# Performance work log

Hardware: AMD Instinct MI355X
Metric: run time of the kernel (lower is better)

## Reference

```python
import jax, jax.numpy as jnp
import numpy as np

# Model dims: batch, seq, d_model, heads, layers, vocab, ffn, max_distance
B, S, D, H, L, V, F, M = 2, 1024, 1024, 16, 6, 32000, 4096, 1024
Dh = D // H


def setup_inputs() -> dict:
    key = jax.random.key(0)
    ks = jax.random.split(key, 24)
    std = 0.02
    w = lambda k, shape: (jax.random.normal(k, shape, jnp.float32) * std)
    return {
        "tokens": jax.random.randint(ks[0], (B, S), 0, V, jnp.int32),
        "emb": w(ks[1], (V, D)),
        "Wq": w(ks[2], (L, D, D)), "bq": jnp.zeros((L, D), jnp.float32),
        "Wk": w(ks[3], (L, D, D)), "bk": jnp.zeros((L, D), jnp.float32),
        "Wv": w(ks[4], (L, D, D)), "bv": jnp.zeros((L, D), jnp.float32),
        "Wo": w(ks[5], (L, D, D)), "bo": jnp.zeros((L, D), jnp.float32),
        "rpe": w(ks[6], (L, M, Dh)),  # per-layer key-RPE embedding table
        "ln1_s": jnp.ones((L, D), jnp.float32), "ln1_b": jnp.zeros((L, D), jnp.float32),
        "ln2_s": jnp.ones((L, D), jnp.float32), "ln2_b": jnp.zeros((L, D), jnp.float32),
        "W1": w(ks[7], (L, D, F)), "b1": jnp.zeros((L, F), jnp.float32),
        "W2": w(ks[8], (L, F, D)), "b2": jnp.zeros((L, D), jnp.float32),
        "Wout": w(ks[9], (D, V)), "bout": jnp.zeros((V,), jnp.float32),
    }


def _ln(x, s, b):
    mu = jnp.mean(x, -1, keepdims=True)
    var = jnp.mean((x - mu) ** 2, -1, keepdims=True)
    return (x - mu) * jax.lax.rsqrt(var + 1e-5) * s + b


def _forward(tokens, emb, Wq, bq, Wk, bk, Wv, bv, Wo, bo, rpe,
             ln1_s, ln1_b, ln2_s, ln2_b, W1, b1, W2, b2, Wout, bout):
    x = emb[tokens]  # (B, S, D); dropout is identity at inference
    mask = jnp.tril(jnp.ones((S, S), bool))
    inv_sqrt_d = np.float32(1.0 / np.sqrt(Dh))

    def block(x, p):
        (wq, bq_, wk, bk_, wv, bv_, wo, bo_, rp,
         l1s, l1b, l2s, l2b, w1, b1_, w2, b2_) = p
        heads = lambda W, b: (x @ W + b).reshape(B, S, H, Dh).transpose(0, 2, 1, 3)
        q, k, v = heads(wq, bq_), heads(wk, bk_), heads(wv, bv_)
        qk = jnp.einsum('bhqd,bhkd->bhqk', q, k)
        # Music-Transformer skew: srel = Q @ E^T, pad-left 1, reshape, drop first row
        srel = jnp.einsum('bhqd,md->bhqm', q, rp[-S:])  # M == S, no clipping branch
        srel = jnp.pad(srel, ((0, 0), (0, 0), (0, 0), (1, 0)))
        srel = srel.reshape(B, H, S + 1, S)[:, :, 1:, :]
        logits = (qk + srel) * inv_sqrt_d
        logits = jnp.where(mask, logits, jnp.float32(-1e9))
        wgt = jax.nn.softmax(logits, axis=-1)
        o = jnp.einsum('bhqk,bhkd->bhqd', wgt, v).transpose(0, 2, 1, 3).reshape(B, S, D)
        o = o @ wo + bo_
        x2 = _ln(x + o, l1s, l1b)           # post-LN residual (attention)
        f = jax.nn.gelu(x2 @ w1 + b1_) @ w2 + b2_
        return _ln(x2 + f, l2s, l2b), None  # post-LN residual (FFN)

    x, _ = jax.lax.scan(block, x, (Wq, bq, Wk, bk, Wv, bv, Wo, bo, rpe,
                                   ln1_s, ln1_b, ln2_s, ln2_b, W1, b1, W2, b2))
    return x @ Wout + bout  # (B, S, V)


def reference(tokens, emb, Wq, bq, Wk, bk, Wv, bv, Wo, bo, rpe,
              ln1_s, ln1_b, ln2_s, ln2_b, W1, b1, W2, b2, Wout, bout):
    return _forward(tokens, emb, Wq, bq, Wk, bk, Wv, bv, Wo, bo, rpe,
                    ln1_s, ln1_b, ln2_s, ln2_b, W1, b1, W2, b2, Wout, bout)
```

## Files before the change

### kernel.cpp

```cpp
#include <hip/hip_runtime.h>
#include <hip/hip_bf16.h>
#include <cstdint>

constexpr int NB = 2, NS = 1024, ND = 1024, NH = 16, NL = 6, NV = 32000, NF = 4096, NDH = 64;

using bf16 = __hip_bfloat16;
typedef __bf16 bf16x8 __attribute__((ext_vector_type(8)));
typedef float f32x4 __attribute__((ext_vector_type(4)));

#define AS1(p) ((const __attribute__((address_space(1))) void*)(p))
#define AS3(p) ((__attribute__((address_space(3))) void*)(p))

__device__ __forceinline__ float gelu_f(float x) {
  float z = 1.5957691216057308f * (x + 0.044715f * x * x * x);
  return x / (1.f + __expf(-z));
}

template<int EP, bool HASBIAS>
__global__ __launch_bounds__(512)
void gemm256p(const bf16* __restrict__ A, const bf16* __restrict__ Bt,
              void* __restrict__ Cv, const float* __restrict__ bias,
              int K, int lda, int ldb, int ldc)
{
  const int nM = gridDim.y, nN = gridDim.x;
  const int nwg = nM * nN;
  const int bid = blockIdx.y * nN + blockIdx.x;
  const int wg = (bid & 7) * (nwg >> 3) + (bid >> 3);
  const int m0 = (wg % nM) * 256;
  const int n0 = (wg / nM) * 256;

  __shared__ char lds[131072];

  const int tid = threadIdx.x, lane = tid & 63, wid = tid >> 6;
  const int wm = (wid >> 2) * 128;
  const int wn = (wid & 3) * 64;
  const int l15 = lane & 15, g4 = lane >> 4;
  const int rdk = (g4 * 16) ^ ((l15 >> 3) << 5);

  const int srow = wid * 16 + (lane >> 2);
  const int scol = ((lane & 3) * 8) ^ (((lane >> 5) & 1) << 4);
  const bf16* gA = A  + (long)(m0 + srow) * lda + scol;
  const bf16* gB = Bt + (long)(n0 + srow) * ldb + scol;
  const long a128 = 128l * lda, b128 = 128l * ldb;

  f32x4 acc[8][4] = {};
  const int NT = K >> 6;

#define SGA(bufsel_, t_, kc_) do {                                                     \
    char* d_ = lds + (bufsel_) * 65536 + (kc_) * 16384 + wid * 1024;                   \
    const long ko_ = (long)(t_) * 64 + (kc_) * 32;                                     \
    __builtin_amdgcn_global_load_lds(AS1(gA + ko_),        AS3(d_),        16, 0, 0);  \
    __builtin_amdgcn_global_load_lds(AS1(gA + ko_ + a128), AS3(d_ + 8192), 16, 0, 0);  \
  } while (0)
#define SGB(bufsel_, t_, kc_) do {                                                     \
    char* d_ = lds + (bufsel_) * 65536 + 32768 + (kc_) * 16384 + wid * 1024;           \
    const long ko_ = (long)(t_) * 64 + (kc_) * 32;                                     \
    __builtin_amdgcn_global_load_lds(AS1(gB + ko_),        AS3(d_),        16, 0, 0);  \
    __builtin_amdgcn_global_load_lds(AS1(gB + ko_ + b128), AS3(d_ + 8192), 16, 0, 0);  \
  } while (0)

#define PH(vm_, bufsel_, kc_, ih_, RDB_, STGX_) do {                                   \
    asm volatile("s_waitcnt vmcnt(" #vm_ ")" ::: "memory");                            \
    __builtin_amdgcn_s_barrier();                                                      \
    asm volatile("" ::: "memory");                                                     \
    const char* la_ = lds + (bufsel_) * 65536 + (kc_) * 16384;                         \
    const char* lb_ = lds + (bufsel_) * 65536 + 32768 + (kc_) * 16384;                 \
    if (RDB_) {                                                                        \
      _Pragma("unroll") for (int j_ = 0; j_ < 4; ++j_)                                 \
        bfr[j_] = *(const bf16x8*)(lb_ + (wn + j_ * 16 + l15) * 64 + rdk);             \
    }                                                                                  \
    bf16x8 af_[4];                                                                     \
    _Pragma("unroll") for (int i2_ = 0; i2_ < 4; ++i2_)                                \
      af_[i2_] = *(const bf16x8*)(la_ + (wm + (ih_) * 64 + i2_ * 16 + l15) * 64 + rdk);\
    STGX_;                                                                             \
    __builtin_amdgcn_s_setprio(1);                                                     \
    _Pragma("unroll") for (int i2_ = 0; i2_ < 4; ++i2_)                                \
      _Pragma("unroll") for (int j_ = 0; j_ < 4; ++j_)                                 \
        acc[(ih_) * 4 + i2_][j_] = __builtin_amdgcn_mfma_f32_16x16x32_bf16(            \
            af_[i2_], bfr[j_], acc[(ih_) * 4 + i2_][j_], 0, 0, 0);                     \
    __builtin_amdgcn_s_setprio(0);                                                     \
    asm volatile("" ::: "memory");                                                     \
    __builtin_amdgcn_s_barrier();                                                      \
  } while (0)

  SGB(0, 0, 0);
  SGA(0, 0, 0);
  SGB(0, 0, 1);
  SGA(0, 0, 1);
  SGB(1, 1, 0);
  SGA(1, 1, 0);
  SGB(1, 1, 1);

  for (int i = 0; i < (NT >> 1) - 1; ++i) {
    const int t1 = 2 * i + 1, t2 = 2 * i + 2, t3 = 2 * i + 3;
    bf16x8 bfr[4];
    PH(10, 0, 0, 0, 1, SGA(1, t1, 1));
    PH(12, 0, 0, 1, 0, SGB(0, t2, 0));
    PH(10, 0, 1, 0, 1, SGA(0, t2, 0));
    PH(12, 0, 1, 1, 0, SGB(0, t2, 1));
    PH(10, 1, 0, 0, 1, SGA(0, t2, 1));
    PH(12, 1, 0, 1, 0, SGB(1, t3, 0));
    PH(10, 1, 1, 0, 1, SGA(1, t3, 0));
    PH(12, 1, 1, 1, 0, SGB(1, t3, 1));
  }
  {
    const int t1 = NT - 1;
    bf16x8 bfr[4];
    PH(10, 0, 0, 0, 1, SGA(1, t1, 1));
    PH(12, 0, 0, 1, 0, (void)0);
    PH( 8, 0, 1, 0, 1, (void)0);
    PH( 8, 0, 1, 1, 0, (void)0);
    PH( 4, 1, 0, 0, 1, (void)0);
    PH( 4, 1, 0, 1, 0, (void)0);
    PH( 0, 1, 1, 0, 1, (void)0);
    PH( 0, 1, 1, 1, 0, (void)0);
  }
#undef PH
#undef SGA
#undef SGB

  const int rq = (lane >> 4) * 4;
  #pragma unroll
  for (int i = 0; i < 8; ++i) {
    const int r0 = m0 + wm + i * 16 + rq;
    #pragma unroll
    for (int j = 0; j < 4; ++j) {
      const int c = n0 + wn + j * 16 + l15;
      float bv = 0.f;
      if constexpr (HASBIAS) bv = bias[c];
      #pragma unroll
      for (int e = 0; e < 4; ++e) {
        float v = acc[i][j][e] + bv;
        if constexpr (EP == 2) v = gelu_f(v);
        if constexpr (EP == 0) ((float*)Cv)[(long)(r0 + e) * ldc + c] = v;
        else                   ((bf16*)Cv)[(long)(r0 + e) * ldc + c] = __float2bfloat16(v);
      }
    }
  }
}

template<int EP, bool HASBIAS, int KSZ>
__global__ __launch_bounds__(256)
void gemm128_bt(const bf16* __restrict__ A, const bf16* __restrict__ Bt,
                void* __restrict__ Cv, const float* __restrict__ bias,
                int K, int lda, int ldb, int ldc, long sEP)
{
  const int nM = gridDim.y, nN = gridDim.x;
  const int nwg = nM * nN;
  const int bid = blockIdx.y * nN + blockIdx.x;
  const int qq = nwg >> 3;
  const int wg = (bid & 7) * qq + (bid >> 3);
  const int m0 = (wg % nM) * 128;
  const int n0 = (wg / nM) * 256;

  const int kLen = K / KSZ;
  const long kOff = (long)blockIdx.z * kLen;

  __shared__ char lds[73728];

  const int tid  = threadIdx.x;
  const int lane = tid & 63;
  const int wid  = tid >> 6;
  const int wn   = wid * 64;
  const int l15  = lane & 15;
  const int rdk  = ((lane >> 4) * 16) ^ ((l15 >> 3) << 5);

  const int srow = wid * 16 + (lane >> 2);
  const int scol = ((lane & 3) * 8) ^ (((lane >> 5) & 1) << 4);
  const bf16* gA = A  + (long)(m0 + srow) * lda + scol + kOff;
  const bf16* gB = Bt + (long)(n0 + srow) * ldb + scol + kOff;
  const long a64 = 64l * lda, b64 = 64l * ldb;

  f32x4 acc[8][4] = {};
  const int NT = kLen >> 5;

#define STG(t_, b_) do {                                                               \
    char* dA = lds + (b_) * 24576 + wid * 1024;                                        \
    char* dB = lds + (b_) * 24576 + 8192 + wid * 1024;                                 \
    const long ko_ = (long)(t_) * 32;                                                  \
    __builtin_amdgcn_global_load_lds(AS1(gA + ko_),           AS3(dA),         16, 0, 0); \
    __builtin_amdgcn_global_load_lds(AS1(gA + ko_ + a64),     AS3(dA + 4096),  16, 0, 0); \
    __builtin_amdgcn_global_load_lds(AS1(gB + ko_),           AS3(dB),         16, 0, 0); \
    __builtin_amdgcn_global_load_lds(AS1(gB + ko_ + b64),     AS3(dB + 4096),  16, 0, 0); \
    __builtin_amdgcn_global_load_lds(AS1(gB + ko_ + 2 * b64), AS3(dB + 8192),  16, 0, 0); \
    __builtin_amdgcn_global_load_lds(AS1(gB + ko_ + 3 * b64), AS3(dB + 12288), 16, 0, 0); \
  } while (0)

#define TBODY(cur_) do {                                                               \
    const char* la_ = lds + (cur_) * 24576;                                            \
    const char* lb_ = la_ + 8192;                                                      \
    bf16x8 bf_[4], af_[8];                                                             \
    _Pragma("unroll") for (int j_ = 0; j_ < 4; ++j_)                                   \
      bf_[j_] = *(const bf16x8*)(lb_ + (wn + j_ * 16 + l15) * 64 + rdk);               \
    _Pragma("unroll") for (int i_ = 0; i_ < 8; ++i_)                                   \
      af_[i_] = *(const bf16x8*)(la_ + (i_ * 16 + l15) * 64 + rdk);                    \
    __builtin_amdgcn_s_setprio(1);                                                     \
    _Pragma("unroll") for (int i_ = 0; i_ < 8; ++i_)                                   \
      _Pragma("unroll") for (int j_ = 0; j_ < 4; ++j_)                                 \
        acc[i_][j_] = __builtin_amdgcn_mfma_f32_16x16x32_bf16(af_[i_], bf_[j_], acc[i_][j_], 0, 0, 0); \
    __builtin_amdgcn_s_setprio(0);                                                     \
  } while (0)

  STG(0, 0); STG(1, 1);
  int cur = 0, nxt = 2;
  for (int t = 0; t < NT - 1; ++t) {
    asm volatile("s_waitcnt vmcnt(6)" ::: "memory");
    __builtin_amdgcn_s_barrier();
    asm volatile("" ::: "memory");
    if (t + 2 < NT) STG(t + 2, nxt);
    TBODY(cur);
    cur = (cur == 2) ? 0 : cur + 1;
    nxt = (nxt == 2) ? 0 : nxt + 1;
  }
  asm volatile("s_waitcnt vmcnt(0)" ::: "memory");
  __builtin_amdgcn_s_barrier();
  asm volatile("" ::: "memory");
  TBODY(cur);
#undef TBODY
#undef STG

  const int rq = (lane >> 4) * 4;
  #pragma unroll
  for (int i = 0; i < 8; ++i) {
    const int r0 = m0 + i * 16 + rq;
    #pragma unroll
    for (int j = 0; j < 4; ++j) {
      const int c = n0 + wn + j * 16 + l15;
      float bv = 0.f;
      if constexpr (HASBIAS) { if (KSZ == 1 || blockIdx.z == 0) bv = bias[c]; }
      #pragma unroll
      for (int e = 0; e < 4; ++e) {
        float v = acc[i][j][e] + bv;
        if constexpr (EP == 0) {
          float* Cz = (float*)Cv + (KSZ > 1 ? (long)blockIdx.z * sEP : 0);
          Cz[(long)(r0 + e) * ldc + c] = v;
        } else if constexpr (EP == 2) {
          ((bf16*)Cv)[(long)(r0 + e) * ldc + c] = __float2bfloat16(gelu_f(v));
        } else {
          ((bf16*)Cv)[(long)(c >> 10) * sEP + (long)(r0 + e) * ND + (c & 1023)] =
              __float2bfloat16(v);
        }
      }
    }
  }
}

template<int BN, int EP, int CZ, bool HASBIAS, int SWZ, int KS>
__global__ __launch_bounds__(256)
void gemm_bt(const bf16* __restrict__ A, const bf16* __restrict__ Bt,
             void* __restrict__ Cv, const float* __restrict__ bias,
             int M, int N, int K, int lda, int ldb, int ldc, int ZH,
             long sAb, long sAh, long sBb, long sBh, long sCb, long sCh, long sBias)
{
  constexpr int BM = 128, BK = 32;
  constexpr int WGN = (BN == 128) ? 2 : 1;
  constexpr int FM  = (BM / (4 / WGN)) / 16;
  constexpr int FN  = (BN / WGN) / 16;

  const int z  = blockIdx.z;
  const int zb = z / ZH, zh = z % ZH;
  const bf16* Ab = A + (long)zb * sAb + (long)zh * sAh;
  const bf16* Bb = Bt + (long)zb * sBb + (long)zh * sBh;

  const int m0 = blockIdx.y * BM;
  const int n0 = blockIdx.x * BN;

  if constexpr (CZ == 3) { if (m0 + n0 + BM + BN - 2 < NS - 1) return; }

  __shared__ bf16 Asm[BM * BK];
  __shared__ bf16 Bsm[BN * BK];

  const int tid  = threadIdx.x;
  const int lane = tid & 63;
  const int wid  = tid >> 6;
  const int wm = (wid / WGN) * (FM * 16);
  const int wn = (wid % WGN) * (FN * 16);
  const int l15 = lane & 15;
  const int lk8 = (lane >> 4) * 8;

  f32x4 acc[FM][FN] = {};

  const int srow = tid >> 2;
  const int scol = (tid & 3) * 8;
  const bf16* gA = Ab + (long)(m0 + srow) * lda + scol;
  const bf16* gB = Bb + (long)(n0 + srow) * ldb + scol;
  bf16* ldsA = Asm + wid * 512;
  bf16* ldsB = Bsm + wid * 512;

  for (int k0 = 0; k0 < K; k0 += BK) {
    __builtin_amdgcn_global_load_lds(AS1(gA + k0), AS3(ldsA), 16, 0, 0);
    __builtin_amdgcn_global_load_lds(AS1(gA + 64l * lda + k0), AS3(ldsA + 2048), 16, 0, 0);
    __builtin_amdgcn_global_load_lds(AS1(gB + k0), AS3(ldsB), 16, 0, 0);
    if constexpr (BN == 128)
      __builtin_amdgcn_global_load_lds(AS1(gB + 64l * ldb + k0), AS3(ldsB + 2048), 16, 0, 0);
    asm volatile("s_waitcnt vmcnt(0)" ::: "memory");
    __syncthreads();

    bf16x8 af[FM], bfr[FN];
    #pragma unroll
    for (int i = 0; i < FM; ++i)
      af[i] = *reinterpret_cast<const bf16x8*>(&Asm[(wm + i * 16 + l15) * BK + lk8]);
    #pragma unroll
    for (int j = 0; j < FN; ++j)
      bfr[j] = *reinterpret_cast<const bf16x8*>(&Bsm[(wn + j * 16 + l15) * BK + lk8]);
    #pragma unroll
    for (int i = 0; i < FM; ++i)
      #pragma unroll
      for (int j = 0; j < FN; ++j)
        acc[i][j] = __builtin_amdgcn_mfma_f32_16x16x32_bf16(af[i], bfr[j], acc[i][j], 0, 0, 0);
    __syncthreads();
  }

  const int rq = (lane >> 4) * 4;
  const long cb = (long)zb * sCb + (long)zh * sCh;
  #pragma unroll
  for (int i = 0; i < FM; ++i) {
    const int r0 = m0 + wm + i * 16 + rq;
    #pragma unroll
    for (int j = 0; j < FN; ++j) {
      const int c = n0 + wn + j * 16 + l15;
      float bv = 0.f;
      if constexpr (HASBIAS) bv = bias[(long)zb * sBias + c];
      #pragma unroll
      for (int e = 0; e < 4; ++e) {
        float v = acc[i][j][e] + bv;
        const long idx = cb + (long)(r0 + e) * ldc + c;
        if constexpr (EP == 0) ((float*)Cv)[idx] = v;
        else                   ((bf16*)Cv)[idx] = __float2bfloat16(v);
      }
    }
  }
}

__global__ __launch_bounds__(256)
void flash_attn_k(const bf16* __restrict__ qkv, const bf16* __restrict__ vt,
                  const bf16* __restrict__ qe, bf16* __restrict__ ob)
{
  const int z  = blockIdx.x;
  const int qt = 15 - blockIdx.y;
  const int b  = z >> 4, h = z & 15;
  const int q0 = qt * 64;
  const int tid  = threadIdx.x;
  const int lane = tid & 63;
  const int wid  = tid >> 6;
  const int l15  = lane & 15;
  const int g4   = lane >> 4;
  const int xk   = (l15 & 7) << 4;

  __shared__ char lds[58368];
  char* Qlds = lds;
  char* Klds = lds + 8192;
  char* Vlds = lds + 24576;
  char* Plds = lds + 40960;

  const bf16* Qg  = qkv + ((long)b * NS + q0) * ND + h * 64;
  const bf16* Kg  = qkv + (long)NB * NS * ND + (long)b * NS * ND + h * 64;
  const bf16* Vg  = vt + (long)z * 64 * NS;
  const bf16* QEg = qe + (long)z * NS * NS;

  #pragma unroll
  for (int i = 0; i < 2; ++i) {
    const int slot = i * 256 + tid;
    const int r = slot >> 3, seg = slot & 7;
    const int sc = (seg ^ (r & 7)) * 8;
    __builtin_amdgcn_global_load_lds(AS1(Qg + (long)r * ND + sc),
                                     AS3(Qlds + (i * 4096 + wid * 1024)), 16, 0, 0);
  }

  f32x4 aqk[8], apv[4];
  #pragma unroll
  for (int j = 0; j < 4; ++j) apv[j] = (f32x4){0.f, 0.f, 0.f, 0.f};
  float mrun[4] = {-3e38f, -3e38f, -3e38f, -3e38f};
  float lrun[4] = {0.f, 0.f, 0.f, 0.f};

  const int nk = (q0 + 191) >> 7;

  for (int kt = 0; kt < nk; ++kt) {
    const int k0 = kt * 128;
    __builtin_amdgcn_s_barrier();

    #pragma unroll
    for (int i = 0; i < 4; ++i) {
      const int slot = i * 256 + tid;
      const int r = slot >> 3, seg = slot & 7;
      const int sc = (seg ^ (r & 7)) * 8;
      __builtin_amdgcn_global_load_lds(AS1(Kg + (long)(k0 + r) * ND + sc),
                                       AS3(Klds + (i * 4096 + wid * 1024)), 16, 0, 0);
    }
    #pragma unroll
    for (int i = 0; i < 4; ++i) {
      const int slot = i * 256 + tid;
      const int d = slot >> 4, seg = slot & 15;
      const int sc = (seg ^ (d & 7)) * 8;
      __builtin_amdgcn_global_load_lds(AS1(Vg + (long)d * NS + k0 + sc),
                                       AS3(Vlds + (i * 4096 + wid * 1024)), 16, 0, 0);
    }

    unsigned short se[4][8];
    #pragma unroll
    for (int e = 0; e < 4; ++e) {
      const int qg = q0 + wid * 16 + g4 * 4 + e;
      const long rowb = (long)qg * NS;
      #pragma unroll
      for (int f = 0; f < 8; ++f) {
        int m = 1023 - qg + k0 + 16 * f + l15;
        m = m > 1023 ? 1023 : m;
        se[e][f] = *(const unsigned short*)(QEg + rowb + m);
      }
    }

    asm volatile("s_waitcnt vmcnt(0)" ::: "memory");
    __builtin_amdgcn_s_barrier();

    #pragma unroll
    for (int f = 0; f < 8; ++f) aqk[f] = (f32x4){0.f, 0.f, 0.f, 0.f};
    #pragma unroll
    for (int ds = 0; ds < 2; ++ds) {
      const int ko = (ds * 32 + g4 * 8) * 2;
      bf16x8 a = *(const bf16x8*)(Qlds + (((wid * 16 + l15) * 128 + ko) ^ xk));
      #pragma unroll
      for (int f = 0; f < 8; ++f) {
        bf16x8 bb = *(const bf16x8*)(Klds + (((16 * f + l15) * 128 + ko) ^ xk));
        aqk[f] = __builtin_amdgcn_mfma_f32_16x16x32_bf16(a, bb, aqk[f], 0, 0, 0);
      }
    }

    float ps[4][8];
    float scl[4];
    #pragma unroll
    for (int e = 0; e < 4; ++e) {
      const int qg = q0 + wid * 16 + g4 * 4 + e;
      float s[8];
      float mx = mrun[e];
      #pragma unroll
      for (int f = 0; f < 8; ++f) {
        const int kg = k0 + 16 * f + l15;
        const float sv = __uint_as_float((unsigned)se[e][f] << 16);
        const float t = (aqk[f][e] + sv) * 0.125f;
        s[f] = (kg <= qg) ? t : -1e30f;
        mx = fmaxf(mx, s[f]);
      }
      #pragma unroll
      for (int o = 1; o < 16; o <<= 1) mx = fmaxf(mx, __shfl_xor(mx, o));
      const float sc_ = __expf(mrun[e] - mx);
      float ls = 0.f;
      #pragma unroll
      for (int f = 0; f < 8; ++f) { const float p = __expf(s[f] - mx); ps[e][f] = p; ls += p; }
      #pragma unroll
      for (int o = 1; o < 16; o <<= 1) ls += __shfl_xor(ls, o);
      lrun[e] = lrun[e] * sc_ + ls;
      mrun[e] = mx;
      scl[e] = sc_;
    }
    #pragma unroll
    for (int fd = 0; fd < 4; ++fd)
      #pragma unroll
      for (int e = 0; e < 4; ++e) apv[fd][e] *= scl[e];

    #pragma unroll
    for (int e = 0; e < 4; ++e) {
      char* pr = Plds + (wid * 16 + g4 * 4 + e) * 272 + l15 * 2;
      #pragma unroll
      for (int f = 0; f < 8; ++f)
        *(bf16*)(pr + f * 32) = __float2bfloat16(ps[e][f]);
    }
    asm volatile("s_waitcnt lgkmcnt(0)" ::: "memory");
    __builtin_amdgcn_sched_barrier(0);

    #pragma unroll
    for (int ks = 0; ks < 4; ++ks) {
      const int ko = (ks * 32 + g4 * 8) * 2;
      bf16x8 a = *(const bf16x8*)(Plds + (wid * 16 + l15) * 272 + ko);
      #pragma unroll
      for (int fd = 0; fd < 4; ++fd) {
        bf16x8 bb = *(const bf16x8*)(Vlds + (((16 * fd + l15) * 256 + ko) ^ xk));
        apv[fd] = __builtin_amdgcn_mfma_f32_16x16x32_bf16(a, bb, apv[fd], 0, 0, 0);
      }
    }
  }

  #pragma unroll
  for (int e = 0; e < 4; ++e) {
    const float rl = 1.f / lrun[e];
    const int qg = q0 + wid * 16 + g4 * 4 + e;
    bf16* orow = ob + ((long)b * NS + qg) * ND + h * 64;
    #pragma unroll
    for (int fd = 0; fd < 4; ++fd)
      orow[16 * fd + l15] = __float2bfloat16(apv[fd][e] * rl);
  }
}

__global__ void transpose64_k(const float* __restrict__ in, bf16* __restrict__ out,
                              int R, int C, long inZ, long outZ) {
  __shared__ float t[64][65];
  const float* ip = in + (long)blockIdx.z * inZ;
  bf16* op = out + (long)blockIdx.z * outZ;
  const int c0 = blockIdx.x * 64, r0 = blockIdx.y * 64;
  const int tid = threadIdx.x;
  const int lr = tid >> 4;
  const int lc = (tid & 15) * 4;
  #pragma unroll
  for (int i = 0; i < 4; ++i) {
    const float4 v = *(const float4*)(ip + (long)(r0 + lr + 16 * i) * C + c0 + lc);
    t[lr + 16 * i][lc]     = v.x;
    t[lr + 16 * i][lc + 1] = v.y;
    t[lr + 16 * i][lc + 2] = v.z;
    t[lr + 16 * i][lc + 3] = v.w;
  }
  __syncthreads();
  #pragma unroll
  for (int i = 0; i < 4; ++i) {
    const int oc = lr + 16 * i;
    ushort4 u;
    bf16 h0 = __float2bfloat16(t[lc][oc]);
    bf16 h1 = __float2bfloat16(t[lc + 1][oc]);
    bf16 h2 = __float2bfloat16(t[lc + 2][oc]);
    bf16 h3 = __float2bfloat16(t[lc + 3][oc]);
    u.x = *(unsigned short*)&h0; u.y = *(unsigned short*)&h1;
    u.z = *(unsigned short*)&h2; u.w = *(unsigned short*)&h3;
    *(ushort4*)(op + (long)(c0 + oc) * R + r0 + lc) = u;
  }
}

__global__ void transpose_v_k(const bf16* __restrict__ v, bf16* __restrict__ vt) {
  __shared__ bf16 t[32][33];
  const int z = blockIdx.z, b = z >> 4, h = z & 15;
  const bf16* ip = v + (long)b * NS * ND + h * 64;
  bf16* op = vt + (long)z * 64 * NS;
  const int s0 = blockIdx.x * 32, d0 = blockIdx.y * 32;
  const int tx = threadIdx.x, ty = threadIdx.y;
  #pragma unroll
  for (int i = 0; i < 4; ++i)
    t[ty * 4 + i][tx] = ip[(long)(s0 + ty * 4 + i) * ND + d0 + tx];
  __syncthreads();
  #pragma unroll
  for (int i = 0; i < 4; ++i)
    op[(long)(d0 + ty * 4 + i) * NS + s0 + tx] = t[tx][ty * 4 + i];
}

__global__ void cvt_bf16_k(const float* __restrict__ in, bf16* __restrict__ out, int n) {
  int i = blockIdx.x * 256 + threadIdx.x;
  if (i < n) out[i] = __float2bfloat16(in[i]);
}

__global__ void pack3_k(const float* __restrict__ a, const float* __restrict__ b,
                        const float* __restrict__ c, float* __restrict__ out) {
  int i = blockIdx.x * 256 + threadIdx.x;
  if (i >= NL * 3 * ND) return;
  int d = i % ND, r = (i / ND) % 3, l = i / (3 * ND);
  const float* src = (r == 0) ? a : ((r == 1) ? b : c);
  out[i] = src[l * ND + d];
}

__global__ void embed_k(const int* __restrict__ tok, const float* __restrict__ emb,
                        float* __restrict__ x, bf16* __restrict__ xb) {
  const int row = blockIdx.x;
  const int t = tok[row];
  const float4 val = ((const float4*)(emb + (long)t * ND))[threadIdx.x];
  ((float4*)(x + (long)row * ND))[threadIdx.x] = val;
  bf16* xp = xb + (long)row * ND + threadIdx.x * 4;
  xp[0] = __float2bfloat16(val.x); xp[1] = __float2bfloat16(val.y);
  xp[2] = __float2bfloat16(val.z); xp[3] = __float2bfloat16(val.w);
}

__global__ void resid_ln_k(float* __restrict__ x, const float* __restrict__ g,
                           long gs,
                           const float* __restrict__ s, const float* __restrict__ b,
                           bf16* __restrict__ xb) {
  const int row = blockIdx.x, tid = threadIdx.x;
  const float4 xv = ((const float4*)(x + (long)row * ND))[tid];
  const float4 ga = ((const float4*)(g + (long)row * ND))[tid];
  const float4 gb = ((const float4*)(g + gs + (long)row * ND))[tid];
  const float4 gc = ((const float4*)(g + 2 * gs + (long)row * ND))[tid];
  const float4 gd = ((const float4*)(g + 3 * gs + (long)row * ND))[tid];
  float h0 = xv.x + ga.x + gb.x + gc.x + gd.x;
  float h1 = xv.y + ga.y + gb.y + gc.y + gd.y;
  float h2 = xv.z + ga.z + gb.z + gc.z + gd.z;
  float h3 = xv.w + ga.w + gb.w + gc.w + gd.w;
  float ls = h0 + h1 + h2 + h3;
  __shared__ float red[8];
  #pragma unroll
  for (int o = 32; o; o >>= 1) ls += __shfl_xor(ls, o);
  const int lane = tid & 63, wid = tid >> 6;
  if (lane == 0) red[wid] = ls;
  __syncthreads();
  const float mu = (red[0] + red[1] + red[2] + red[3]) * (1.f / ND);
  const float d0 = h0 - mu, d1 = h1 - mu, d2 = h2 - mu, d3 = h3 - mu;
  float lv = d0 * d0 + d1 * d1 + d2 * d2 + d3 * d3;
  #pragma unroll
  for (int o = 32; o; o >>= 1) lv += __shfl_xor(lv, o);
  if (lane == 0) red[4 + wid] = lv;
  __syncthreads();
  const float rs = rsqrtf((red[4] + red[5] + red[6] + red[7]) * (1.f / ND) + 1e-5f);
  const float4 sv = ((const float4*)s)[tid];
  const float4 bv = ((const float4*)b)[tid];
  const float y0 = d0 * rs * sv.x + bv.x, y1 = d1 * rs * sv.y + bv.y;
  const float y2 = d2 * rs * sv.z + bv.z, y3 = d3 * rs * sv.w + bv.w;
  ((float4*)(x + (long)row * ND))[tid] = make_float4(y0, y1, y2, y3);
  bf16* xp = xb + (long)row * ND + tid * 4;
  xp[0] = __float2bfloat16(y0); xp[1] = __float2bfloat16(y1);
  xp[2] = __float2bfloat16(y2); xp[3] = __float2bfloat16(y3);
}

extern "C" void kernel_launch(void* const* d_in, const int* in_sizes, int n_in,
                              void* d_out, int out_size, void* d_ws, size_t ws_size,
                              hipStream_t stream) {
  const int*   tokens = (const int*)d_in[0];
  const float* emb  = (const float*)d_in[1];
  const float* Wq   = (const float*)d_in[2];
  const float* bq   = (const float*)d_in[3];
  const float* Wk   = (const float*)d_in[4];
  const float* bk   = (const float*)d_in[5];
  const float* Wv   = (const float*)d_in[6];
  const float* bv   = (const float*)d_in[7];
  const float* Wo   = (const float*)d_in[8];
  const float* bo   = (const float*)d_in[9];
  const float* rpe  = (const float*)d_in[10];
  const float* ln1s = (const float*)d_in[11];
  const float* ln1b = (const float*)d_in[12];
  const float* ln2s = (const float*)d_in[13];
  const float* ln2b = (const float*)d_in[14];
  const float* W1   = (const float*)d_in[15];
  const float* b1   = (const float*)d_in[16];
  const float* W2   = (const float*)d_in[17];
  const float* b2   = (const float*)d_in[18];
  const float* Wout = (const float*)d_in[19];
  const float* bout = (const float*)d_in[20];
  float* out = (float*)d_out;

  char* wsb = (char*)d_ws;
  size_t off = 0;
  auto take = [&](size_t bytes) -> void* {
    void* r = wsb + off;
    off = (off + bytes + 255) & ~(size_t)255;
    return r;
  };
  bf16*  wqkvT = (bf16*)take((size_t)NL * 3 * ND * ND * 2);
  bf16*  woT   = (bf16*)take((size_t)NL * ND * ND * 2);
  bf16*  w1T   = (bf16*)take((size_t)NL * NF * ND * 2);
  bf16*  w2T   = (bf16*)take((size_t)NL * ND * NF * 2);
  bf16*  woutT = (bf16*)take((size_t)NV * ND * 2);
  bf16*  rpeb  = (bf16*)take((size_t)NL * NS * NDH * 2);
  float* qkvb  = (float*)take((size_t)NL * 3 * ND * 4);
  float* x     = (float*)take((size_t)NB * NS * ND * 4);
  bf16*  xb    = (bf16*)take((size_t)NB * NS * ND * 2);
  bf16*  qkv   = (bf16*)take((size_t)3 * NB * NS * ND * 2);
  bf16*  vt    = (bf16*)take((size_t)NB * NS * ND * 2);
  bf16*  ob    = (bf16*)take((size_t)NB * NS * ND * 2);
  float* g     = (float*)take((size_t)4 * NB * NS * ND * 4);
  bf16*  hbuf  = (bf16*)take((size_t)NB * NS * NF * 2);
  bf16*  qe    = (bf16*)take((size_t)NB * NH * NS * NS * 2 + 4096);
  (void)in_sizes; (void)n_in; (void)out_size; (void)ws_size;

  const long gStride = (long)NB * NS * ND;

  transpose64_k<<<dim3(ND/64, ND/64, NL), 256, 0, stream>>>(Wq, wqkvT,                   ND, ND, (long)ND*ND, (long)3*ND*ND);
  transpose64_k<<<dim3(ND/64, ND/64, NL), 256, 0, stream>>>(Wk, wqkvT + (size_t)ND*ND,   ND, ND, (long)ND*ND, (long)3*ND*ND);
  transpose64_k<<<dim3(ND/64, ND/64, NL), 256, 0, stream>>>(Wv, wqkvT + (size_t)2*ND*ND, ND, ND, (long)ND*ND, (long)3*ND*ND);
  transpose64_k<<<dim3(ND/64, ND/64, NL), 256, 0, stream>>>(Wo, woT,                     ND, ND, (long)ND*ND, (long)ND*ND);
  transpose64_k<<<dim3(NF/64, ND/64, NL), 256, 0, stream>>>(W1, w1T,                     ND, NF, (long)ND*NF, (long)NF*ND);
  transpose64_k<<<dim3(ND/64, NF/64, NL), 256, 0, stream>>>(W2, w2T,                     NF, ND, (long)NF*ND, (long)ND*NF);
  transpose64_k<<<dim3(NV/64, ND/64, 1),  256, 0, stream>>>(Wout, woutT,                 ND, NV, 0, 0);
  cvt_bf16_k<<<(NL*NS*NDH + 255)/256, 256, 0, stream>>>(rpe, rpeb, NL*NS*NDH);
  pack3_k<<<(NL*3*ND + 255)/256, 256, 0, stream>>>(bq, bk, bv, qkvb);
  embed_k<<<NB*NS, 256, 0, stream>>>(tokens, emb, x, xb);

  const dim3 tb(32, 8);
  for (int l = 0; l < NL; ++l) {
    gemm128_bt<3, true, 1><<<dim3(3*ND/256, NB*NS/128), 256, 0, stream>>>(
        xb, wqkvT + (size_t)l*3*ND*ND, qkv, qkvb + (size_t)l*3*ND,
        ND, ND, ND, ND, gStride);
    transpose_v_k<<<dim3(NS/32, 2, NB*NH), tb, 0, stream>>>(qkv + (size_t)2*NB*NS*ND, vt);
    gemm_bt<128, 1, 3, false, 0, 0><<<dim3(NS/128, NS/128, NB*NH), 256, 0, stream>>>(
        qkv, rpeb + (size_t)l*NS*NDH, qe, nullptr,
        NS, NS, NDH, ND, NDH, NS, NH,
        (long)NS*ND, 64, 0, 0, (long)NH*NS*NS, (long)NS*NS, 0);
    flash_attn_k<<<dim3(NB*NH, 16), 256, 0, stream>>>(qkv, vt, qe, ob);
    gemm128_bt<0, true, 4><<<dim3(ND/256, NB*NS/128, 4), 256, 0, stream>>>(
        ob, woT + (size_t)l*ND*ND, g, bo + (size_t)l*ND, ND, ND, ND, ND, gStride);
    resid_ln_k<<<NB*NS, 256, 0, stream>>>(x, g, gStride,
        ln1s + (size_t)l*ND, ln1b + (size_t)l*ND, xb);
    gemm128_bt<2, true, 1><<<dim3(NF/256, NB*NS/128), 256, 0, stream>>>(
        xb, w1T + (size_t)l*NF*ND, hbuf, b1 + (size_t)l*NF, ND, ND, ND, NF, 0);
    gemm128_bt<0, true, 4><<<dim3(ND/256, NB*NS/128, 4), 256, 0, stream>>>(
        hbuf, w2T + (size_t)l*ND*NF, g, b2 + (size_t)l*ND, NF, NF, NF, ND, gStride);
    resid_ln_k<<<NB*NS, 256, 0, stream>>>(x, g, gStride,
        ln2s + (size_t)l*ND, ln2b + (size_t)l*ND, xb);
  }
  gemm256p<0, true><<<dim3(NV/256, NB*NS/256), 512, 0, stream>>>(
      xb, woutT, out, bout, ND, ND, ND, NV);
}
```

Before: 1.358 ms.

## Restructure GEMM into 4-stage K pipeline and register-prefetch attention K/V tiles

The main GEMM moves from a double-buffered, 8-phase 64-wide K schedule to a 4-slot ring of 32-wide K stages. Each stage loads all A and B fragments, issues the prefetch three stages ahead, and splits the MFMAs across lgkmcnt waits with one barrier per stage. The flash attention kernel now keeps Q in registers instead of LDS and prefetches the next K/V tile into registers during the current iteration, then writes it to swizzled LDS. The aim is better overlap of global loads with compute and fewer barriers, at the cost of more registers and different LDS usage.

```diff
diff --git a/kernel.cpp b/kernel.cpp
--- a/kernel.cpp
+++ b/kernel.cpp
@@ -44,80 +44,56 @@
   const long a128 = 128l * lda, b128 = 128l * ldb;
 
   f32x4 acc[8][4] = {};
-  const int NT = K >> 6;
-
-#define SGA(bufsel_, t_, kc_) do {                                                     \
-    char* d_ = lds + (bufsel_) * 65536 + (kc_) * 16384 + wid * 1024;                   \
-    const long ko_ = (long)(t_) * 64 + (kc_) * 32;                                     \
-    __builtin_amdgcn_global_load_lds(AS1(gA + ko_),        AS3(d_),        16, 0, 0);  \
-    __builtin_amdgcn_global_load_lds(AS1(gA + ko_ + a128), AS3(d_ + 8192), 16, 0, 0);  \
+  const int NP = K >> 5;
+
+#define STGP(p_) do {                                                                  \
+    const int s_ = (p_) & 3; const long ko_ = (long)(p_) * 32;                         \
+    char* dA = lds + s_ * 32768 + wid * 1024;                                          \
+    char* dB = dA + 16384;                                                             \
+    __builtin_amdgcn_global_load_lds(AS1(gA + ko_),        AS3(dA),        16, 0, 0);  \
+    __builtin_amdgcn_global_load_lds(AS1(gA + ko_ + a128), AS3(dA + 8192), 16, 0, 0);  \
+    __builtin_amdgcn_global_load_lds(AS1(gB + ko_),        AS3(dB),        16, 0, 0);  \
+    __builtin_amdgcn_global_load_lds(AS1(gB + ko_ + b128), AS3(dB + 8192), 16, 0, 0);  \
   } while (0)
-#define SGB(bufsel_, t_, kc_) do {                                                     \
-    char* d_ = lds + (bufsel_) * 65536 + 32768 + (kc_) * 16384 + wid * 1024;           \
-    const long ko_ = (long)(t_) * 64 + (kc_) * 32;                                     \
-    __builtin_amdgcn_global_load_lds(AS1(gB + ko_),        AS3(d_),        16, 0, 0);  \
-    __builtin_amdgcn_global_load_lds(AS1(gB + ko_ + b128), AS3(d_ + 8192), 16, 0, 0);  \
-  } while (0)
-
-#define PH(vm_, bufsel_, kc_, ih_, RDB_, STGX_) do {                                   \
+
+#define PAIR(vm_, p_, DOSTG_) do {                                                     \
     asm volatile("s_waitcnt vmcnt(" #vm_ ")" ::: "memory");                            \
     __builtin_amdgcn_s_barrier();                                                      \
     asm volatile("" ::: "memory");                                                     \
-    const char* la_ = lds + (bufsel_) * 65536 + (kc_) * 16384;                         \
-    const char* lb_ = lds + (bufsel_) * 65536 + 32768 + (kc_) * 16384;                 \
-    if (RDB_) {                                                                        \
+    const char* la_ = lds + ((p_) & 3) * 32768;                                        \
+    const char* lb_ = la_ + 16384;                                                     \
+    bf16x8 bfr[4], af[8];                                                              \
+    _Pragma("unroll") for (int j_ = 0; j_ < 4; ++j_)                                   \
+      bfr[j_] = *(const bf16x8*)(lb_ + (wn + j_ * 16 + l15) * 64 + rdk);               \
+    _Pragma("unroll") for (int i_ = 0; i_ < 4; ++i_)                                   \
+      af[i_] = *(const bf16x8*)(la_ + (wm + i_ * 16 + l15) * 64 + rdk);                \
+    __builtin_amdgcn_sched_barrier(0);                                                 \
+    _Pragma("unroll") for (int i_ = 4; i_ < 8; ++i_)                                   \
+      af[i_] = *(const bf16x8*)(la_ + (wm + i_ * 16 + l15) * 64 + rdk);                \
+    if (DOSTG_) STGP((p_) + 3);                                                        \
+    asm volatile("s_waitcnt lgkmcnt(4)" ::: "memory");                                 \
+    __builtin_amdgcn_sched_barrier(0);                                                 \
+    __builtin_amdgcn_s_setprio(1);                                                     \
+    _Pragma("unroll") for (int i_ = 0; i_ < 4; ++i_)                                   \
       _Pragma("unroll") for (int j_ = 0; j_ < 4; ++j_)                                 \
-        bfr[j_] = *(const bf16x8*)(lb_ + (wn + j_ * 16 + l15) * 64 + rdk);             \
-    }                                                                                  \
-    bf16x8 af_[4];                                                                     \
-    _Pragma("unroll") for (int i2_ = 0; i2_ < 4; ++i2_)                                \
-      af_[i2_] = *(const bf16x8*)(la_ + (wm + (ih_) * 64 + i2_ * 16 + l15) * 64 + rdk);\
-    STGX_;                                                                             \
+        acc[i_][j_] = __builtin_amdgcn_mfma_f32_16x16x32_bf16(af[i_], bfr[j_], acc[i_][j_], 0, 0, 0); \
+    __builtin_amdgcn_s_setprio(0);                                                     \
+    asm volatile("s_waitcnt lgkmcnt(0)" ::: "memory");                                 \
+    __builtin_amdgcn_sched_barrier(0);                                                 \
     __builtin_amdgcn_s_setprio(1);                                                     \
-    _Pragma("unroll") for (int i2_ = 0; i2_ < 4; ++i2_)                                \
+    _Pragma("unroll") for (int i_ = 4; i_ < 8; ++i_)                                   \
       _Pragma("unroll") for (int j_ = 0; j_ < 4; ++j_)                                 \
-        acc[(ih_) * 4 + i2_][j_] = __builtin_amdgcn_mfma_f32_16x16x32_bf16(            \
-            af_[i2_], bfr[j_], acc[(ih_) * 4 + i2_][j_], 0, 0, 0);                     \
+        acc[i_][j_] = __builtin_amdgcn_mfma_f32_16x16x32_bf16(af[i_], bfr[j_], acc[i_][j_], 0, 0, 0); \
     __builtin_amdgcn_s_setprio(0);                                                     \
-    asm volatile("" ::: "memory");                                                     \
-    __builtin_amdgcn_s_barrier();                                                      \
   } while (0)
 
-  SGB(0, 0, 0);
-  SGA(0, 0, 0);
-  SGB(0, 0, 1);
-  SGA(0, 0, 1);
-  SGB(1, 1, 0);
-  SGA(1, 1, 0);
-  SGB(1, 1, 1);
-
-  for (int i = 0; i < (NT >> 1) - 1; ++i) {
-    const int t1 = 2 * i + 1, t2 = 2 * i + 2, t3 = 2 * i + 3;
-    bf16x8 bfr[4];
-    PH(10, 0, 0, 0, 1, SGA(1, t1, 1));
-    PH(12, 0, 0, 1, 0, SGB(0, t2, 0));
-    PH(10, 0, 1, 0, 1, SGA(0, t2, 0));
-    PH(12, 0, 1, 1, 0, SGB(0, t2, 1));
-    PH(10, 1, 0, 0, 1, SGA(0, t2, 1));
-    PH(12, 1, 0, 1, 0, SGB(1, t3, 0));
-    PH(10, 1, 1, 0, 1, SGA(1, t3, 0));
-    PH(12, 1, 1, 1, 0, SGB(1, t3, 1));
-  }
-  {
-    const int t1 = NT - 1;
-    bf16x8 bfr[4];
-    PH(10, 0, 0, 0, 1, SGA(1, t1, 1));
-    PH(12, 0, 0, 1, 0, (void)0);
-    PH( 8, 0, 1, 0, 1, (void)0);
-    PH( 8, 0, 1, 1, 0, (void)0);
-    PH( 4, 1, 0, 0, 1, (void)0);
-    PH( 4, 1, 0, 1, 0, (void)0);
-    PH( 0, 1, 1, 0, 1, (void)0);
-    PH( 0, 1, 1, 1, 0, (void)0);
-  }
-#undef PH
-#undef SGA
-#undef SGB
+  STGP(0); STGP(1); STGP(2);
+  for (int p = 0; p < NP - 3; ++p) PAIR(8, p, 1);
+  PAIR(8, NP - 3, 0);
+  PAIR(4, NP - 2, 0);
+  PAIR(0, NP - 1, 0);
+#undef PAIR
+#undef STGP
 
   const int rq = (lane >> 4) * 4;
   #pragma unroll
@@ -347,24 +323,28 @@
   const int g4   = lane >> 4;
   const int xk   = (l15 & 7) << 4;
 
-  __shared__ char lds[58368];
-  char* Qlds = lds;
-  char* Klds = lds + 8192;
-  char* Vlds = lds + 24576;
-  char* Plds = lds + 40960;
-
-  const bf16* Qg  = qkv + ((long)b * NS + q0) * ND + h * 64;
+  __shared__ char lds[50176];
+  char* Klds = lds;
+  char* Vlds = lds + 16384;
+  char* Plds = lds + 32768;
+
   const bf16* Kg  = qkv + (long)NB * NS * ND + (long)b * NS * ND + h * 64;
   const bf16* Vg  = vt + (long)z * 64 * NS;
   const bf16* QEg = qe + (long)z * NS * NS;
 
-  #pragma unroll
-  for (int i = 0; i < 2; ++i) {
-    const int slot = i * 256 + tid;
-    const int r = slot >> 3, seg = slot & 7;
-    const int sc = (seg ^ (r & 7)) * 8;
-    __builtin_amdgcn_global_load_lds(AS1(Qg + (long)r * ND + sc),
-                                     AS3(Qlds + (i * 4096 + wid * 1024)), 16, 0, 0);
+  const bf16* Qrow = qkv + ((long)b * NS + q0 + wid * 16 + l15) * ND + h * 64 + g4 * 8;
+  const bf16x8 qr0 = *(const bf16x8*)(Qrow);
+  const bf16x8 qr1 = *(const bf16x8*)(Qrow + 32);
+
+  const int kR = tid >> 3, kSeg = tid & 7;
+  const int vD = tid >> 4, vSeg = tid & 15;
+  int wKa[4], wVa[4];
+  #pragma unroll
+  for (int i = 0; i < 4; ++i) {
+    const int r = i * 32 + kR;
+    wKa[i] = (r * 128 + kSeg * 16) ^ ((r & 7) << 4);
+    const int d = i * 16 + vD;
+    wVa[i] = (d * 256 + vSeg * 16) ^ ((d & 7) << 4);
   }
 
   f32x4 aqk[8], apv[4];
@@ -375,26 +355,21 @@
 
   const int nk = (q0 + 191) >> 7;
 
+  bf16x8 kr[4], vr[4];
+  #pragma unroll
+  for (int i = 0; i < 4; ++i) {
+    kr[i] = *(const bf16x8*)(Kg + (long)(i * 32 + kR) * ND + kSeg * 8);
+    vr[i] = *(const bf16x8*)(Vg + (long)(i * 16 + vD) * NS + vSeg * 8);
+  }
+
   for (int kt = 0; kt < nk; ++kt) {
     const int k0 = kt * 128;
     __builtin_amdgcn_s_barrier();
 
     #pragma unroll
-    for (int i = 0; i < 4; ++i) {
-      const int slot = i * 256 + tid;
-      const int r = slot >> 3, seg = slot & 7;
-      const int sc = (seg ^ (r & 7)) * 8;
-      __builtin_amdgcn_global_load_lds(AS1(Kg + (long)(k0 + r) * ND + sc),
-                                       AS3(Klds + (i * 4096 + wid * 1024)), 16, 0, 0);
-    }
-    #pragma unroll
-    for (int i = 0; i < 4; ++i) {
-      const int slot = i * 256 + tid;
-      const int d = slot >> 4, seg = slot & 15;
-      const int sc = (seg ^ (d & 7)) * 8;
-      __builtin_amdgcn_global_load_lds(AS1(Vg + (long)d * NS + k0 + sc),
-                                       AS3(Vlds + (i * 4096 + wid * 1024)), 16, 0, 0);
-    }
+    for (int i = 0; i < 4; ++i) *(bf16x8*)(Klds + wKa[i]) = kr[i];
+    #pragma unroll
+    for (int i = 0; i < 4; ++i) *(bf16x8*)(Vlds + wVa[i]) = vr[i];
 
     unsigned short se[4][8];
     #pragma unroll
@@ -408,20 +383,33 @@
         se[e][f] = *(const unsigned short*)(QEg + rowb + m);
       }
     }
-
-    asm volatile("s_waitcnt vmcnt(0)" ::: "memory");
+    __builtin_amdgcn_sched_barrier(0);
+    if (kt + 1 < nk) {
+      const int k1 = k0 + 128;
+      #pragma unroll
+      for (int i = 0; i < 4; ++i) {
+        kr[i] = *(const bf16x8*)(Kg + (long)(k1 + i * 32 + kR) * ND + kSeg * 8);
+        vr[i] = *(const bf16x8*)(Vg + (long)(i * 16 + vD) * NS + k1 + vSeg * 8);
+      }
+    }
+    asm volatile("s_waitcnt lgkmcnt(0)" ::: "memory");
+    __builtin_amdgcn_sched_barrier(0);
     __builtin_amdgcn_s_barrier();
 
     #pragma unroll
     for (int f = 0; f < 8; ++f) aqk[f] = (f32x4){0.f, 0.f, 0.f, 0.f};
-    #pragma unroll
-    for (int ds = 0; ds < 2; ++ds) {
-      const int ko = (ds * 32 + g4 * 8) * 2;
-      bf16x8 a = *(const bf16x8*)(Qlds + (((wid * 16 + l15) * 128 + ko) ^ xk));
+    {
+      const int ko0 = g4 * 16;
       #pragma unroll
       for (int f = 0; f < 8; ++f) {
-        bf16x8 bb = *(const bf16x8*)(Klds + (((16 * f + l15) * 128 + ko) ^ xk));
-        aqk[f] = __builtin_amdgcn_mfma_f32_16x16x32_bf16(a, bb, aqk[f], 0, 0, 0);
+        bf16x8 bb = *(const bf16x8*)(Klds + (((16 * f + l15) * 128 + ko0) ^ xk));
+        aqk[f] = __builtin_amdgcn_mfma_f32_16x16x32_bf16(qr0, bb, aqk[f], 0, 0, 0);
+      }
+      const int ko1 = 64 + g4 * 16;
+      #pragma unroll
+      for (int f = 0; f < 8; ++f) {
+        bf16x8 bb = *(const bf16x8*)(Klds + (((16 * f + l15) * 128 + ko1) ^ xk));
+        aqk[f] = __builtin_amdgcn_mfma_f32_16x16x32_bf16(qr1, bb, aqk[f], 0, 0, 0);
       }
     }
 
```

Measured after the change: 1.355 ms. About the same (-0.2%).
